# Optimization experiments

Hardware: AMD Instinct MI355X
Metric: run time of the kernel (lower is better)

The kernel has to match this reference:

```python
import jax, jax.numpy as jnp
import numpy as np

B, C, H, W = 2, 256, 64, 64
HEADS, DIM_HEAD = 8, 64
INNER = HEADS * DIM_HEAD


def setup_inputs() -> dict:
    key = jax.random.key(0)
    k1, k2, k3, k4 = jax.random.split(key, 4)
    x = jax.random.normal(k1, (B, C, H, W), dtype=jnp.float32)
    # 1x1 conv weights stored as [out_ch, in_ch]
    w_qkv = jax.random.normal(k2, (3 * INNER, C), dtype=jnp.float32) * (1.0 / np.sqrt(C))
    w_out = jax.random.normal(k3, (C, INNER), dtype=jnp.float32) * (1.0 / np.sqrt(INNER))
    b_out = jax.random.normal(k4, (C,), dtype=jnp.float32) * 0.01
    return {"x": x, "w_qkv": w_qkv, "w_out": w_out, "b_out": b_out}


def reference(x, w_qkv, w_out, b_out):
    b, c, h, w = x.shape
    n = h * w
    # 1x1 conv == channel matmul
    qkv = jnp.einsum('oc,bchw->bohw', w_qkv, x)  # [B, 3*inner, H, W]
    qkv = qkv.reshape(b, 3, HEADS, DIM_HEAD, n)
    qkv = jnp.transpose(qkv, (1, 0, 2, 4, 3))    # [3, B, heads, N, dim_head]
    q, k, v = qkv[0], qkv[1], qkv[2]
    scale = 1.0 / (DIM_HEAD ** 0.5)
    dots = jnp.einsum('bhnd,bhmd->bhnm', q, k) * scale  # [B, heads, N, N]
    attn = jax.nn.softmax(dots, axis=-1)
    out = jnp.einsum('bhnm,bhmd->bhnd', attn, v)        # [B, heads, N, dim_head]
    out = jnp.transpose(out, (0, 1, 3, 2)).reshape(b, INNER, h, w)
    return jnp.einsum('ci,bihw->bchw', w_out, out) + b_out[None, :, None, None]
```

## Files before the change

kernel.cpp:

```cpp
#include <hip/hip_runtime.h>
#include <hip/hip_bf16.h>

typedef unsigned short u16;
typedef __attribute__((ext_vector_type(8))) short bf16x8;
typedef __attribute__((ext_vector_type(4))) float f32x4;
typedef __attribute__((ext_vector_type(8))) unsigned short u16x8;
typedef __attribute__((ext_vector_type(4))) unsigned short u16x4;

#define N_POS 4096
#define HEADS 8
#define DHEAD 64
#define CIN   256
#define INNER 512
#define NSPLIT 2
#define JCHUNK (N_POS / NSPLIT)

__device__ __forceinline__ u16 f2bf(float f) {
    union { float f; unsigned int u; } v; v.f = f;
    unsigned int u = v.u + 0x7FFFu + ((v.u >> 16) & 1u);
    return (u16)(u >> 16);
}

__device__ __forceinline__ float bf2f(u16 h) {
    union { float f; unsigned int u; } v; v.u = ((unsigned int)h) << 16;
    return v.f;
}

__device__ __forceinline__ unsigned int pkbf2(float lo, float hi) {
    union { __hip_bfloat162 b; unsigned int u; } cv;
    cv.b = __float22bfloat162_rn(make_float2(lo, hi));
    return cv.u;
}

__global__ __launch_bounds__(256) void k0_prep(const float* __restrict__ x,
                                               const float* __restrict__ w_qkv,
                                               const float* __restrict__ w_out,
                                               u16* __restrict__ xT,
                                               u16* __restrict__ wq,
                                               u16* __restrict__ wo) {
    int bid = blockIdx.x;
    int t   = threadIdx.x;
    if (bid < 256) {
        int b = bid >> 7, rest = bid & 127;
        int n  = (rest & 15) * 256 + t;
        int c0 = (rest >> 4) * 32;
        const float* xp = x + (size_t)b * CIN * N_POS + n;
        u16* op = xT + ((size_t)(b * N_POS + n)) * CIN + c0;
        for (int g = 0; g < 4; ++g) {
            u16x8 v;
            for (int j = 0; j < 8; ++j)
                v[j] = f2bf(xp[(size_t)(c0 + g * 8 + j) * N_POS]);
            *(u16x8*)(op + g * 8) = v;
        }
    } else if (bid < 448) {
        size_t idx = (size_t)(bid - 256) * 2048 + t * 8;
        u16x8 v;
        for (int j = 0; j < 8; ++j) v[j] = f2bf(w_qkv[idx + j]);
        *(u16x8*)(wq + idx) = v;
    } else {
        size_t idx = (size_t)(bid - 448) * 2048 + t * 8;
        u16x8 v;
        for (int j = 0; j < 8; ++j) v[j] = f2bf(w_out[idx + j]);
        *(u16x8*)(wo + idx) = v;
    }
}

__global__ __launch_bounds__(256, 4) void k1_qkv(const u16* __restrict__ wq,
                                                 const u16* __restrict__ xT,
                                                 u16* __restrict__ q_ws,
                                                 u16* __restrict__ k_ws,
                                                 u16* __restrict__ vt_ws) {
    __shared__ u16 Alds[64 * 40];
    __shared__ u16 Blds[128 * 40];
    int tid = threadIdx.x;
    int n0  = blockIdx.x * 128;
    int by  = blockIdx.y;
    int b   = blockIdx.z;
    int o0  = by * 64;
    int sel = by >> 3;
    int h   = by & 7;
    int wv = tid >> 6, l = tid & 63, quad = l >> 4, l15 = l & 15;
    int srow = tid >> 2, sseg = tid & 3;
    int brow = tid >> 1, bseg = tid & 1;

    f32x4 acc[8] = {};
    for (int c0 = 0; c0 < CIN; c0 += 32) {
        *(u16x8*)&Alds[srow * 40 + sseg * 8] =
            *(const u16x8*)(wq + (size_t)(o0 + srow) * CIN + c0 + sseg * 8);
        const u16* xp = xT + ((size_t)(b * N_POS + n0 + brow)) * CIN + c0 + bseg * 16;
        *(u16x8*)&Blds[brow * 40 + bseg * 16]     = *(const u16x8*)xp;
        *(u16x8*)&Blds[brow * 40 + bseg * 16 + 8] = *(const u16x8*)(xp + 8);
        __syncthreads();
        bf16x8 af = *(const bf16x8*)&Alds[(wv * 16 + l15) * 40 + quad * 8];
        if (sel < 2) {
            for (int nt = 0; nt < 8; ++nt) {
                bf16x8 bfrag = *(const bf16x8*)&Blds[(nt * 16 + l15) * 40 + quad * 8];
                acc[nt] = __builtin_amdgcn_mfma_f32_16x16x32_bf16(af, bfrag, acc[nt], 0, 0, 0);
            }
        } else {
            for (int nt = 0; nt < 8; ++nt) {
                bf16x8 bfrag = *(const bf16x8*)&Blds[(nt * 16 + l15) * 40 + quad * 8];
                acc[nt] = __builtin_amdgcn_mfma_f32_16x16x32_bf16(bfrag, af, acc[nt], 0, 0, 0);
            }
        }
        __syncthreads();
    }
    const float QSCALE = 0.125f * 1.44269504088896f;
    int bh = b * HEADS + h;
    if (sel < 2) {
        float sc = (sel == 0) ? QSCALE : 1.0f;
        u16* base = (sel == 0) ? q_ws : k_ws;
        int dbase = wv * 16 + quad * 4;
        for (int nt = 0; nt < 8; ++nt) {
            int n = n0 + nt * 16 + l15;
            u16x4 pk;
            for (int r = 0; r < 4; ++r) pk[r] = f2bf(acc[nt][r] * sc);
            *(u16x4*)&base[((size_t)bh * N_POS + n) * DHEAD + dbase] = pk;
        }
    } else {
        int dloc = wv * 16 + l15;
        for (int nt = 0; nt < 8; ++nt) {
            u16x4 pk;
            for (int r = 0; r < 4; ++r) pk[r] = f2bf(acc[nt][r]);
            *(u16x4*)&vt_ws[((size_t)bh * DHEAD + dloc) * N_POS
                            + n0 + nt * 16 + quad * 4] = pk;
        }
    }
}

__global__ __launch_bounds__(256, 2) void k2_attn(const u16* __restrict__ q_ws,
                                                  const u16* __restrict__ k_ws,
                                                  const u16* __restrict__ vt_ws,
                                                  u16* __restrict__ op_ws,
                                                  float* __restrict__ lw_ws) {
    __shared__ u16 Klds[2][64 * 72];
    __shared__ u16 Vlds[2][64 * 72];
    int tid = threadIdx.x;
    int v   = blockIdx.x + (blockIdx.y << 4) + (blockIdx.z << 8);
    int slot = v & 7, idx = v >> 3;
    int bh   = slot * 2 + (idx & 1);
    int q0   = ((idx >> 1) & 15) * 256;
    int half = idx >> 5;
    int jbase = half * JCHUNK;
    int wv = tid >> 6, l = tid & 63, quad = l >> 4, l15 = l & 15;
    int srow = tid >> 2, sseg = tid & 3;
    int srowp = (srow & 0x23) | ((srow & 4) << 2) | ((srow & 0x18) >> 1);
    int kofs = srowp * 72 + sseg * 16;
    int vofs = srow * 72 + sseg * 16;

    const u16* qp = q_ws + ((size_t)(bh * N_POS + q0 + wv * 64 + l15)) * DHEAD + quad * 8;
    bf16x8 bq[4][2];
    for (int it = 0; it < 4; ++it) {
        bq[it][0] = *(const bf16x8*)(qp + (size_t)it * 16 * DHEAD);
        bq[it][1] = *(const bf16x8*)(qp + (size_t)it * 16 * DHEAD + 32);
    }

    f32x4 Oacc[4][4] = {};
    float lsum[4] = {0.f, 0.f, 0.f, 0.f};

    const u16* kp = k_ws + ((size_t)(bh * N_POS + srow)) * DHEAD + sseg * 16;
    const u16* vp = vt_ws + ((size_t)(bh * DHEAD + srow)) * N_POS + sseg * 16;

    u16x8 pf0 = *(const u16x8*)(kp + (size_t)jbase * DHEAD);
    u16x8 pf1 = *(const u16x8*)(kp + (size_t)jbase * DHEAD + 8);
    u16x8 pf2 = *(const u16x8*)(vp + jbase);
    u16x8 pf3 = *(const u16x8*)(vp + jbase + 8);
    *(u16x8*)&Klds[0][kofs]     = pf0;
    *(u16x8*)&Klds[0][kofs + 8] = pf1;
    *(u16x8*)&Vlds[0][vofs]     = pf2;
    *(u16x8*)&Vlds[0][vofs + 8] = pf3;
    {
        const u16* kpj = kp + (size_t)(jbase + 64) * DHEAD;
        pf0 = *(const u16x8*)kpj;
        pf1 = *(const u16x8*)(kpj + 8);
        pf2 = *(const u16x8*)(vp + jbase + 64);
        pf3 = *(const u16x8*)(vp + jbase + 72);
    }
    __syncthreads();

    int cur = 0;
    for (int j0 = jbase; j0 < jbase + JCHUNK; j0 += 64) {
        if (j0 + 64 < jbase + JCHUNK) {
            *(u16x8*)&Klds[cur ^ 1][kofs]     = pf0;
            *(u16x8*)&Klds[cur ^ 1][kofs + 8] = pf1;
            *(u16x8*)&Vlds[cur ^ 1][vofs]     = pf2;
            *(u16x8*)&Vlds[cur ^ 1][vofs + 8] = pf3;
        }

        union PF { unsigned int u[4]; bf16x8 v; };
        PF pfr[4][2];
        for (int p = 0; p < 2; ++p)
            for (int a = 0; a < 2; ++a) {
                const u16* kb = &Klds[cur][((2 * p + a) * 16 + l15) * 72 + quad * 8];
                bf16x8 kf0 = *(const bf16x8*)kb;
                bf16x8 kf1 = *(const bf16x8*)(kb + 32);
                f32x4 z[4];
                __builtin_amdgcn_s_setprio(1);
                for (int it = 0; it < 4; ++it) {
                    f32x4 t = {};
                    t = __builtin_amdgcn_mfma_f32_16x16x32_bf16(kf0, bq[it][0], t, 0, 0, 0);
                    t = __builtin_amdgcn_mfma_f32_16x16x32_bf16(kf1, bq[it][1], t, 0, 0, 0);
                    z[it] = t;
                }
                __builtin_amdgcn_s_setprio(0);
                for (int it = 0; it < 4; ++it) {
                    float e0 = __builtin_amdgcn_exp2f(z[it][0]);
                    float e1 = __builtin_amdgcn_exp2f(z[it][1]);
                    float e2 = __builtin_amdgcn_exp2f(z[it][2]);
                    float e3 = __builtin_amdgcn_exp2f(z[it][3]);
                    lsum[it] += (e0 + e1) + (e2 + e3);
                    pfr[it][p].u[2 * a]     = pkbf2(e0, e1);
                    pfr[it][p].u[2 * a + 1] = pkbf2(e2, e3);
                }
            }

        __builtin_amdgcn_s_setprio(1);
        for (int dt = 0; dt < 4; ++dt)
            for (int p = 0; p < 2; ++p) {
                bf16x8 vf = *(const bf16x8*)&Vlds[cur][(dt * 16 + l15) * 72 + p * 32 + quad * 8];
                for (int it = 0; it < 4; ++it)
                    Oacc[it][dt] = __builtin_amdgcn_mfma_f32_16x16x32_bf16(vf, pfr[it][p].v, Oacc[it][dt], 0, 0, 0);
            }
        __builtin_amdgcn_s_setprio(0);

        if (j0 + 128 < jbase + JCHUNK) {
            const u16* kpj = kp + (size_t)(j0 + 128) * DHEAD;
            pf0 = *(const u16x8*)kpj;
            pf1 = *(const u16x8*)(kpj + 8);
            pf2 = *(const u16x8*)(vp + j0 + 128);
            pf3 = *(const u16x8*)(vp + j0 + 136);
        }
        __syncthreads();
        cur ^= 1;
    }

    int b = bh >> 3, h = bh & 7;
    u16* opb = op_ws + (size_t)half * 2 * N_POS * INNER;
    float* lwb = lw_ws + (size_t)half * 2 * HEADS * N_POS;
    for (int it = 0; it < 4; ++it) {
        float ls = lsum[it];
        ls += __shfl_xor(ls, 16);
        ls += __shfl_xor(ls, 32);
        int n = q0 + wv * 64 + it * 16 + l15;
        if (quad == 0) lwb[(size_t)bh * N_POS + n] = ls;
        u16* dst = opb + ((size_t)(b * N_POS + n)) * INNER + h * DHEAD;
        for (int dt = 0; dt < 4; ++dt) {
            u16x4 pk;
            for (int r = 0; r < 4; ++r) pk[r] = f2bf(Oacc[it][dt][r]);
            *(u16x4*)&dst[dt * 16 + quad * 4] = pk;
        }
    }
}

__global__ __launch_bounds__(512) void k3_out(const u16* __restrict__ wo,
                                              const float* __restrict__ b_out,
                                              const u16* __restrict__ op_ws,
                                              const float* __restrict__ lw_ws,
                                              float* __restrict__ out) {
    __shared__ u16 Alds[256 * 40];
    __shared__ u16 Blds[32 * 40];
    int tid = threadIdx.x;
    int n0 = blockIdx.x * 32;
    int b  = blockIdx.y;
    int wv = tid >> 6, l = tid & 63, quad = l >> 4, l15 = l & 15;

    f32x4 acc[2][2] = {};
    for (int i0 = 0; i0 < INNER; i0 += 32) {
        {
            int row = tid >> 1, seg = tid & 1;
            const u16* src = wo + (size_t)row * INNER + i0 + seg * 16;
            *(u16x8*)&Alds[row * 40 + seg * 16]     = *(const u16x8*)src;
            *(u16x8*)&Alds[row * 40 + seg * 16 + 8] = *(const u16x8*)(src + 8);
        }
        if (tid < 128) {
            int srow = tid >> 2, sseg = tid & 3;
            int i = i0 + sseg * 8;
            int h = i >> 6;
            int n = n0 + srow;
            size_t lidx = ((size_t)(b * HEADS + h)) * N_POS + n;
            float ls = lw_ws[lidx] + lw_ws[(size_t)2 * HEADS * N_POS + lidx];
            float inv = 1.0f / ls;
            size_t oidx = ((size_t)(b * N_POS + n)) * INNER + i;
            u16x8 pv0 = *(const u16x8*)(op_ws + oidx);
            u16x8 pv1 = *(const u16x8*)(op_ws + (size_t)2 * N_POS * INNER + oidx);
            u16x8 vv;
            for (int k = 0; k < 8; ++k)
                vv[k] = f2bf((bf2f(pv0[k]) + bf2f(pv1[k])) * inv);
            *(u16x8*)&Blds[srow * 40 + sseg * 8] = vv;
        }
        __syncthreads();
        for (int ac = 0; ac < 2; ++ac) {
            bf16x8 af = *(const bf16x8*)&Alds[(wv * 32 + ac * 16 + l15) * 40 + quad * 8];
            for (int nt = 0; nt < 2; ++nt) {
                bf16x8 bfrag = *(const bf16x8*)&Blds[(nt * 16 + l15) * 40 + quad * 8];
                acc[ac][nt] = __builtin_amdgcn_mfma_f32_16x16x32_bf16(af, bfrag, acc[ac][nt], 0, 0, 0);
            }
        }
        __syncthreads();
    }
    for (int ac = 0; ac < 2; ++ac)
        for (int r = 0; r < 4; ++r) {
            int c = wv * 32 + ac * 16 + quad * 4 + r;
            float bias = b_out[c];
            for (int nt = 0; nt < 2; ++nt) {
                int n = n0 + nt * 16 + l15;
                out[((size_t)(b * CIN + c)) * N_POS + n] = acc[ac][nt][r] + bias;
            }
        }
}

extern "C" void kernel_launch(void* const* d_in, const int* in_sizes, int n_in,
                              void* d_out, int out_size, void* d_ws, size_t ws_size,
                              hipStream_t stream) {
    const float* x     = (const float*)d_in[0];
    const float* w_qkv = (const float*)d_in[1];
    const float* w_out = (const float*)d_in[2];
    const float* b_out = (const float*)d_in[3];
    float* out = (float*)d_out;

    u16* ws    = (u16*)d_ws;
    u16* xT    = ws;
    u16* q_ws  = xT   + (size_t)2 * N_POS * CIN;
    u16* k_ws  = q_ws + (size_t)2 * HEADS * N_POS * DHEAD;
    u16* vt_ws = k_ws + (size_t)2 * HEADS * N_POS * DHEAD;
    u16* wq_bf = vt_ws + (size_t)2 * HEADS * N_POS * DHEAD;
    u16* wo_bf = wq_bf + (size_t)3 * INNER * CIN;
    u16* op_ws = wo_bf + (size_t)CIN * INNER;
    float* lw_ws = (float*)(op_ws + (size_t)NSPLIT * 2 * N_POS * INNER);

    hipLaunchKernelGGL(k0_prep, dim3(512), dim3(256), 0, stream,
                       x, w_qkv, w_out, xT, wq_bf, wo_bf);
    hipLaunchKernelGGL(k1_qkv, dim3(32, 24, 2), dim3(256), 0, stream,
                       wq_bf, xT, q_ws, k_ws, vt_ws);
    hipLaunchKernelGGL(k2_attn, dim3(16, 16, NSPLIT), dim3(256), 0, stream,
                       q_ws, k_ws, vt_ws, op_ws, lw_ws);
    hipLaunchKernelGGL(k3_out, dim3(128, 2), dim3(512), 0, stream,
                       wo_bf, b_out, op_ws, lw_ws, out);
}
```

Before: 178.1 us.

## Widen QKV projection tile and restructure output projection with double-buffered weights

The QKV projection kernel now gives each block 256 positions instead of 128, doubling accumulators per wave and halving the grid. The intent is better reuse of the weight tile per block. The output projection kernel now handles 16 positions per block. It merges the two split-attention partials for all 512 inner channels once into LDS, then streams the weight tiles through a double buffer with a single barrier per step. This removes the repeated partial-merge work and one barrier per iteration, but each block now does less MFMA work relative to the weight traffic it loads, and the larger QKV tile raises register pressure.

```diff
diff --git a/kernel.cpp b/kernel.cpp
--- a/kernel.cpp
+++ b/kernel.cpp
@@ -65,15 +65,15 @@
     }
 }
 
-__global__ __launch_bounds__(256, 4) void k1_qkv(const u16* __restrict__ wq,
+__global__ __launch_bounds__(256, 2) void k1_qkv(const u16* __restrict__ wq,
                                                  const u16* __restrict__ xT,
                                                  u16* __restrict__ q_ws,
                                                  u16* __restrict__ k_ws,
                                                  u16* __restrict__ vt_ws) {
     __shared__ u16 Alds[64 * 40];
-    __shared__ u16 Blds[128 * 40];
+    __shared__ u16 Blds[256 * 40];
     int tid = threadIdx.x;
-    int n0  = blockIdx.x * 128;
+    int n0  = blockIdx.x * 256;
     int by  = blockIdx.y;
     int b   = blockIdx.z;
     int o0  = by * 64;
@@ -81,24 +81,26 @@
     int h   = by & 7;
     int wv = tid >> 6, l = tid & 63, quad = l >> 4, l15 = l & 15;
     int srow = tid >> 2, sseg = tid & 3;
-    int brow = tid >> 1, bseg = tid & 1;
-
-    f32x4 acc[8] = {};
+
+    f32x4 acc[16] = {};
     for (int c0 = 0; c0 < CIN; c0 += 32) {
         *(u16x8*)&Alds[srow * 40 + sseg * 8] =
             *(const u16x8*)(wq + (size_t)(o0 + srow) * CIN + c0 + sseg * 8);
-        const u16* xp = xT + ((size_t)(b * N_POS + n0 + brow)) * CIN + c0 + bseg * 16;
-        *(u16x8*)&Blds[brow * 40 + bseg * 16]     = *(const u16x8*)xp;
-        *(u16x8*)&Blds[brow * 40 + bseg * 16 + 8] = *(const u16x8*)(xp + 8);
+        const u16* xp = xT + ((size_t)(b * N_POS + n0 + tid)) * CIN + c0;
+        u16* bd = &Blds[tid * 40];
+        *(u16x8*)(bd)      = *(const u16x8*)(xp);
+        *(u16x8*)(bd + 8)  = *(const u16x8*)(xp + 8);
+        *(u16x8*)(bd + 16) = *(const u16x8*)(xp + 16);
+        *(u16x8*)(bd + 24) = *(const u16x8*)(xp + 24);
         __syncthreads();
         bf16x8 af = *(const bf16x8*)&Alds[(wv * 16 + l15) * 40 + quad * 8];
         if (sel < 2) {
-            for (int nt = 0; nt < 8; ++nt) {
+            for (int nt = 0; nt < 16; ++nt) {
                 bf16x8 bfrag = *(const bf16x8*)&Blds[(nt * 16 + l15) * 40 + quad * 8];
                 acc[nt] = __builtin_amdgcn_mfma_f32_16x16x32_bf16(af, bfrag, acc[nt], 0, 0, 0);
             }
         } else {
-            for (int nt = 0; nt < 8; ++nt) {
+            for (int nt = 0; nt < 16; ++nt) {
                 bf16x8 bfrag = *(const bf16x8*)&Blds[(nt * 16 + l15) * 40 + quad * 8];
                 acc[nt] = __builtin_amdgcn_mfma_f32_16x16x32_bf16(bfrag, af, acc[nt], 0, 0, 0);
             }
@@ -111,7 +113,7 @@
         float sc = (sel == 0) ? QSCALE : 1.0f;
         u16* base = (sel == 0) ? q_ws : k_ws;
         int dbase = wv * 16 + quad * 4;
-        for (int nt = 0; nt < 8; ++nt) {
+        for (int nt = 0; nt < 16; ++nt) {
             int n = n0 + nt * 16 + l15;
             u16x4 pk;
             for (int r = 0; r < 4; ++r) pk[r] = f2bf(acc[nt][r] * sc);
@@ -119,7 +121,7 @@
         }
     } else {
         int dloc = wv * 16 + l15;
-        for (int nt = 0; nt < 8; ++nt) {
+        for (int nt = 0; nt < 16; ++nt) {
             u16x4 pk;
             for (int r = 0; r < 4; ++r) pk[r] = f2bf(acc[nt][r]);
             *(u16x4*)&vt_ws[((size_t)bh * DHEAD + dloc) * N_POS
@@ -257,55 +259,60 @@
                                               const u16* __restrict__ op_ws,
                                               const float* __restrict__ lw_ws,
                                               float* __restrict__ out) {
-    __shared__ u16 Alds[256 * 40];
-    __shared__ u16 Blds[32 * 40];
+    __shared__ u16 Alds[2][256 * 36];
+    __shared__ u16 Blds[16 * 520];
     int tid = threadIdx.x;
-    int n0 = blockIdx.x * 32;
+    int n0 = blockIdx.x * 16;
     int b  = blockIdx.y;
     int wv = tid >> 6, l = tid & 63, quad = l >> 4, l15 = l & 15;
 
-    f32x4 acc[2][2] = {};
-    for (int i0 = 0; i0 < INNER; i0 += 32) {
-        {
-            int row = tid >> 1, seg = tid & 1;
-            const u16* src = wo + (size_t)row * INNER + i0 + seg * 16;
-            *(u16x8*)&Alds[row * 40 + seg * 16]     = *(const u16x8*)src;
-            *(u16x8*)&Alds[row * 40 + seg * 16 + 8] = *(const u16x8*)(src + 8);
-        }
-        if (tid < 128) {
-            int srow = tid >> 2, sseg = tid & 3;
-            int i = i0 + sseg * 8;
-            int h = i >> 6;
-            int n = n0 + srow;
+    {
+        int i8 = tid & 63;
+        int h  = i8 >> 3;
+        for (int p = 0; p < 2; ++p) {
+            int nl = p * 8 + (tid >> 6);
+            int n = n0 + nl;
             size_t lidx = ((size_t)(b * HEADS + h)) * N_POS + n;
             float ls = lw_ws[lidx] + lw_ws[(size_t)2 * HEADS * N_POS + lidx];
             float inv = 1.0f / ls;
-            size_t oidx = ((size_t)(b * N_POS + n)) * INNER + i;
+            size_t oidx = ((size_t)(b * N_POS + n)) * INNER + i8 * 8;
             u16x8 pv0 = *(const u16x8*)(op_ws + oidx);
             u16x8 pv1 = *(const u16x8*)(op_ws + (size_t)2 * N_POS * INNER + oidx);
             u16x8 vv;
             for (int k = 0; k < 8; ++k)
                 vv[k] = f2bf((bf2f(pv0[k]) + bf2f(pv1[k])) * inv);
-            *(u16x8*)&Blds[srow * 40 + sseg * 8] = vv;
+            *(u16x8*)&Blds[nl * 520 + i8 * 8] = vv;
+        }
+    }
+    {
+        int row = tid >> 1, seg = tid & 1;
+        const u16* src = wo + (size_t)row * INNER + seg * 16;
+        *(u16x8*)&Alds[0][row * 36 + seg * 16]     = *(const u16x8*)src;
+        *(u16x8*)&Alds[0][row * 36 + seg * 16 + 8] = *(const u16x8*)(src + 8);
+    }
+    __syncthreads();
+
+    f32x4 acc[2] = {};
+    int cur = 0;
+    for (int s = 0; s < 16; ++s) {
+        if (s + 1 < 16) {
+            int row = tid >> 1, seg = tid & 1;
+            const u16* src = wo + (size_t)row * INNER + (s + 1) * 32 + seg * 16;
+            *(u16x8*)&Alds[cur ^ 1][row * 36 + seg * 16]     = *(const u16x8*)src;
+            *(u16x8*)&Alds[cur ^ 1][row * 36 + seg * 16 + 8] = *(const u16x8*)(src + 8);
+        }
+        for (int ac = 0; ac < 2; ++ac) {
+            bf16x8 af = *(const bf16x8*)&Alds[cur][(wv * 32 + ac * 16 + l15) * 36 + quad * 8];
+            bf16x8 bfrag = *(const bf16x8*)&Blds[l15 * 520 + s * 32 + quad * 8];
+            acc[ac] = __builtin_amdgcn_mfma_f32_16x16x32_bf16(af, bfrag, acc[ac], 0, 0, 0);
         }
         __syncthreads();
-        for (int ac = 0; ac < 2; ++ac) {
-            bf16x8 af = *(const bf16x8*)&Alds[(wv * 32 + ac * 16 + l15) * 40 + quad * 8];
-            for (int nt = 0; nt < 2; ++nt) {
-                bf16x8 bfrag = *(const bf16x8*)&Blds[(nt * 16 + l15) * 40 + quad * 8];
-                acc[ac][nt] = __builtin_amdgcn_mfma_f32_16x16x32_bf16(af, bfrag, acc[ac][nt], 0, 0, 0);
-            }
-        }
-        __syncthreads();
+        cur ^= 1;
     }
     for (int ac = 0; ac < 2; ++ac)
         for (int r = 0; r < 4; ++r) {
             int c = wv * 32 + ac * 16 + quad * 4 + r;
-            float bias = b_out[c];
-            for (int nt = 0; nt < 2; ++nt) {
-                int n = n0 + nt * 16 + l15;
-                out[((size_t)(b * CIN + c)) * N_POS + n] = acc[ac][nt][r] + bias;
-            }
+            out[((size_t)(b * CIN + c)) * N_POS + n0 + l15] = acc[ac][r] + b_out[c];
         }
 }
 
@@ -330,10 +337,10 @@
 
     hipLaunchKernelGGL(k0_prep, dim3(512), dim3(256), 0, stream,
                        x, w_qkv, w_out, xT, wq_bf, wo_bf);
-    hipLaunchKernelGGL(k1_qkv, dim3(32, 24, 2), dim3(256), 0, stream,
+    hipLaunchKernelGGL(k1_qkv, dim3(16, 24, 2), dim3(256), 0, stream,
                        wq_bf, xT, q_ws, k_ws, vt_ws);
     hipLaunchKernelGGL(k2_attn, dim3(16, 16, NSPLIT), dim3(256), 0, stream,
                        q_ws, k_ws, vt_ws, op_ws, lw_ws);
-    hipLaunchKernelGGL(k3_out, dim3(128, 2), dim3(512), 0, stream,
+    hipLaunchKernelGGL(k3_out, dim3(256, 2), dim3(512), 0, stream,
                        wo_bf, b_out, op_ws, lw_ws, out);
 }
```

New measurement: 178.5 us. No clear change (+0.2%).
